# Performance work log

Measured on AMD Instinct MI355X. Metric: run time of the kernel, lower is better.

## Reference

```python
import jax, jax.numpy as jnp
import numpy as np

B, DIM, H, W, NH, WS = 128, 768, 16, 16, 12, 16
N = H * W  # 256, equals window_size**2


def setup_inputs() -> dict:
    key = jax.random.key(0)
    ks = jax.random.split(key, 8)
    s = 0.02  # small init scale for params
    return {
        "x": jax.random.normal(ks[0], (B, DIM, H, W), dtype=jnp.float32),
        "face_priors": jax.random.uniform(ks[1], (B, N, N), dtype=jnp.float32),
        "qkv_w": jax.random.normal(ks[2], (3 * DIM, DIM), dtype=jnp.float32) * s,
        "qkv_b": jax.random.normal(ks[3], (3 * DIM,), dtype=jnp.float32) * s,
        "rel_table": jax.random.normal(ks[4], ((2 * WS - 1) * (2 * WS - 1), NH), dtype=jnp.float32) * s,
        "face_prior": jax.random.normal(ks[5], (1, NH, N, N), dtype=jnp.float32) * s,
        "proj_w": jax.random.normal(ks[6], (DIM, DIM), dtype=jnp.float32) * s,
        "proj_b": jax.random.normal(ks[7], (DIM,), dtype=jnp.float32) * s,
    }


def _relative_position_bias(rel_table, h, w):
    # Static index computation (h, w are Python ints under jit).
    coords = jnp.stack(jnp.meshgrid(jnp.arange(h), jnp.arange(w), indexing="ij"))  # [2,h,w]
    flat = coords.reshape(2, -1)                     # [2, N]
    rel = flat[:, :, None] - flat[:, None, :]        # [2, N, N]
    idx = (rel[0] + h - 1) * (2 * w - 1) + (rel[1] + w - 1)  # [N, N]
    return rel_table[idx].transpose(2, 0, 1)         # [nh, N, N]


def reference(x, face_priors, qkv_w, qkv_b, rel_table, face_prior, proj_w, proj_b):
    b, c, h, w = x.shape
    n = h * w
    nh = face_prior.shape[1]
    hd = c // nh
    scale = hd ** -0.5

    x_flat = x.reshape(b, c, n).transpose(0, 2, 1)   # [B, N, C]
    qkv = (x_flat @ qkv_w.T + qkv_b).reshape(b, n, 3, nh, hd).transpose(2, 0, 3, 1, 4)
    q, k, v = qkv[0], qkv[1], qkv[2]                 # each [B, nh, N, hd]

    attn = jnp.einsum("bhnd,bhmd->bhnm", q, k) * scale
    attn = attn + face_prior + _relative_position_bias(rel_table, h, w)[None]
    attn = attn * face_priors[:, None]               # broadcast over heads
    attn = jax.nn.softmax(attn, axis=-1)

    out = jnp.einsum("bhnm,bhmd->bhnd", attn, v)     # [B, nh, N, hd]
    out = out.transpose(0, 2, 1, 3).reshape(b, n, c)
    out = out @ proj_w.T + proj_b                    # [B, N, C]
    return out.transpose(0, 2, 1).reshape(b, c, h, w)
```

## Files before the change

### kernel.cpp

```cpp
#include <hip/hip_runtime.h>

#define B_   128
#define DIM_ 768
#define NH_  12
#define HD_  64
#define N_   256

using half8 = __attribute__((ext_vector_type(8))) _Float16;
using half4 = __attribute__((ext_vector_type(4))) _Float16;
using f32x4 = __attribute__((ext_vector_type(4))) float;
typedef unsigned short u16;
typedef unsigned int   u32;

#define GLDS16(srcp, dstp) \
    __builtin_amdgcn_global_load_lds( \
        (const __attribute__((address_space(1))) void*)(srcp), \
        (__attribute__((address_space(3))) void*)(dstp), 16, 0, 0)

__device__ __forceinline__ int xcd_chunked(int orig, int nwg) {
    int xcd = orig & 7, loc = orig >> 3;
    int qq = nwg >> 3, rr = nwg & 7;
    return (xcd < rr ? xcd * (qq + 1) : rr * (qq + 1) + (xcd - rr) * qq) + loc;
}

__global__ __launch_bounds__(256) void bias16_kernel(
    const float* __restrict__ face_prior, const float* __restrict__ rel_table,
    _Float16* __restrict__ b16)
{
    int gid = blockIdx.x * 256 + threadIdx.x;
    int idx = gid * 2;
    union { _Float16 s[2]; u32 u; } P;
    #pragma unroll
    for (int j = 0; j < 2; ++j) {
        int id = idx + j;
        int m = id & 255;
        int n = (id >> 8) & 255;
        int h = id >> 16;
        int rn = n >> 4, cn = n & 15;
        int rm = m >> 4, cm = m & 15;
        int ridx = (rn - rm + 15) * 31 + (cn - cm + 15);
        P.s[j] = (_Float16)(face_prior[id] + rel_table[ridx * NH_ + h]);
    }
    *(u32*)(b16 + idx) = P.u;
}

__global__ __launch_bounds__(256) void conv_f32_f16(
    const float* __restrict__ in, _Float16* __restrict__ o16, int n8)
{
    int i = blockIdx.x * 256 + threadIdx.x;
    if (i >= n8) return;
    float4 a = *(const float4*)(in + (size_t)i * 8);
    float4 b = *(const float4*)(in + (size_t)i * 8 + 4);
    float v[8] = {a.x, a.y, a.z, a.w, b.x, b.y, b.z, b.w};
    union { _Float16 s[8]; uint4 q; } H;
    #pragma unroll
    for (int j = 0; j < 8; ++j) H.s[j] = (_Float16)v[j];
    *(uint4*)(o16 + (size_t)i * 8) = H.q;
}

__global__ __launch_bounds__(256) void conv_w_f16_staged(
    const float* __restrict__ in, _Float16* __restrict__ o16, int nchunk)
{
    int gid = blockIdx.x * 256 + threadIdx.x;
    if (gid >= nchunk) return;
    int t   = gid / 12288;
    int rem = gid % 12288;
    int ks  = rem >> 9;
    int c   = rem & 511;
    int mtb = c >> 6, kgrp = (c >> 4) & 3, r16 = c & 15;
    int srow = t * 128 + mtb * 16 + r16;
    int sk   = ks * 32 + kgrp * 8;
    float4 a = *(const float4*)(in + (size_t)srow * DIM_ + sk);
    float4 b = *(const float4*)(in + (size_t)srow * DIM_ + sk + 4);
    float v[8] = {a.x, a.y, a.z, a.w, b.x, b.y, b.z, b.w};
    union { _Float16 s[8]; uint4 q; } H;
    #pragma unroll
    for (int j = 0; j < 8; ++j) H.s[j] = (_Float16)v[j];
    *(uint4*)(o16 + (size_t)gid * 8) = H.q;
}

__global__ __launch_bounds__(256) void conv_qw_staged(
    const float* __restrict__ in, _Float16* __restrict__ o16, int nchunk)
{
    int gid = blockIdx.x * 256 + threadIdx.x;
    if (gid >= nchunk) return;
    int t   = gid / 24576;
    int rem = gid % 24576;
    int ks  = rem >> 10;
    int c   = rem & 1023;
    int mtb = c >> 6, kg = (c >> 4) & 3, r16 = c & 15;
    int srow = t * 256 + mtb * 16 + r16;
    int sk   = ks * 32 + kg * 8;
    float4 a = *(const float4*)(in + (size_t)srow * DIM_ + sk);
    float4 b = *(const float4*)(in + (size_t)srow * DIM_ + sk + 4);
    float v[8] = {a.x, a.y, a.z, a.w, b.x, b.y, b.z, b.w};
    union { _Float16 s[8]; uint4 q; } H;
    #pragma unroll
    for (int j = 0; j < 8; ++j) H.s[j] = (_Float16)v[j];
    *(uint4*)(o16 + (size_t)gid * 8) = H.q;
}

__global__ __launch_bounds__(256) void conv_transpose_x_f16(
    const float* __restrict__ x, _Float16* __restrict__ xa)
{
    __shared__ float T[64][65];
    const int b = blockIdx.z, k0 = blockIdx.x * 64, n0 = blockIdx.y * 64;
    const int t = threadIdx.x;
    const float* xb = x + (size_t)b * DIM_ * N_;
    {
        int nn = t & 63, kg = t >> 6;
        #pragma unroll
        for (int r = 0; r < 16; ++r) {
            int kk = r * 4 + kg;
            T[kk][nn] = xb[(size_t)(k0 + kk) * N_ + n0 + nn];
        }
    }
    __syncthreads();
    {
        int kk2 = (t & 31) * 2, ng = t >> 5;
        #pragma unroll
        for (int r = 0; r < 8; ++r) {
            int nn = r * 8 + ng;
            union { _Float16 s[2]; u32 u; } P;
            P.s[0] = (_Float16)T[kk2][nn];
            P.s[1] = (_Float16)T[kk2 + 1][nn];
            int n = n0 + nn, k = k0 + kk2;
            int ks = k >> 5, kg = (k >> 3) & 3, koff = k & 7;
            int mtb = n >> 4, r16 = n & 15;
            size_t o = (((size_t)b * 24 + ks) * 1024
                        + mtb * 64 + kg * 16 + r16) * 8 + koff;
            *(u32*)(xa + o) = P.u;
        }
    }
}

__global__ __launch_bounds__(512) void qkv_gemm(
    const _Float16* __restrict__ w16, const _Float16* __restrict__ x16,
    const float* __restrict__ bvec,
    _Float16* __restrict__ q16, _Float16* __restrict__ k16,
    _Float16* __restrict__ v16,
    int b0, int cb)
{
    extern __shared__ _Float16 lds[];

    const int tid  = threadIdx.x;
    const int lane = tid & 63;
    const int wv   = tid >> 6;
    const int wr   = wv >> 2;
    const int wc   = wv & 3;

    const int wg = xcd_chunked(blockIdx.x, cb * 9);
    const int by = wg % 9;
    const int bl = wg / 9;
    const int b  = b0 + bl;

    const _Float16* wbase = w16 + (size_t)by * 24 * 8192;
    const _Float16* xbase = x16 + (size_t)b  * 24 * 8192;

    f32x4 acc[8][4];
    #pragma unroll
    for (int i = 0; i < 8; ++i)
        #pragma unroll
        for (int j = 0; j < 4; ++j)
            acc[i][j] = (f32x4){0.f, 0.f, 0.f, 0.f};

    const int sbase = wv * 512;

#define STAGE_T(tt, slot) do { \
        const _Float16* ws_ = wbase + (size_t)(tt) * 8192; \
        const _Float16* xs_ = xbase + (size_t)(tt) * 8192; \
        _Float16* da_ = lds + (slot) * 8192; \
        _Float16* db_ = lds + 24576 + (slot) * 8192; \
        GLDS16(ws_ + sbase + lane * 8,        da_ + sbase); \
        GLDS16(ws_ + 4096 + sbase + lane * 8, da_ + 4096 + sbase); \
        GLDS16(xs_ + sbase + lane * 8,        db_ + sbase); \
        GLDS16(xs_ + 4096 + sbase + lane * 8, db_ + 4096 + sbase); \
    } while (0)

    STAGE_T(0, 0); STAGE_T(1, 1); STAGE_T(2, 2);

    int slot = 0;
    for (int t = 0; t < 24; ++t) {
        if (t < 22)       asm volatile("s_waitcnt vmcnt(8)" ::: "memory");
        else if (t == 22) asm volatile("s_waitcnt vmcnt(4)" ::: "memory");
        else              asm volatile("s_waitcnt vmcnt(0)" ::: "memory");
        __builtin_amdgcn_s_barrier();

        const _Float16* SAs = lds + slot * 8192;
        const _Float16* SBs = lds + 24576 + slot * 8192;
        half8 af[8];
        #pragma unroll
        for (int mt = 0; mt < 8; ++mt)
            af[mt] = *(const half8*)&SAs[((wr * 8 + mt) * 64 + lane) * 8];
        #pragma unroll
        for (int nt = 0; nt < 4; ++nt) {
            half8 bf = *(const half8*)&SBs[((wc * 4 + nt) * 64 + lane) * 8];
            #pragma unroll
            for (int mt = 0; mt < 8; ++mt)
                acc[mt][nt] = __builtin_amdgcn_mfma_f32_16x16x32_f16(af[mt], bf, acc[mt][nt], 0, 0, 0);
        }
        __builtin_amdgcn_s_barrier();

        if (t + 3 < 24) STAGE_T(t + 3, slot);
        slot = (slot == 2) ? 0 : slot + 1;
    }
#undef STAGE_T

    const int which = by / 3;
    _Float16* slab = (which == 0) ? q16 : (which == 1) ? k16 : v16;
    const int ocr0 = (by % 3) * 256 + wr * 128 + ((lane >> 4) << 2);
    const int nb   = wc * 64 + (lane & 15);

    #pragma unroll
    for (int mt = 0; mt < 8; ++mt) {
        int oc_in = ocr0 + mt * 16;
        float4 bv = *(const float4*)(bvec + which * DIM_ + oc_in);
        int hh = oc_in >> 6, d = oc_in & 63;
        size_t rowbase = ((size_t)bl * NH_ + hh) * (size_t)(N_ * HD_) + d;
        #pragma unroll
        for (int nt = 0; nt < 4; ++nt) {
            int n = nb + nt * 16;
            union { _Float16 s[4]; uint2 u; } H;
            H.s[0] = (_Float16)(acc[mt][nt][0] + bv.x);
            H.s[1] = (_Float16)(acc[mt][nt][1] + bv.y);
            H.s[2] = (_Float16)(acc[mt][nt][2] + bv.z);
            H.s[3] = (_Float16)(acc[mt][nt][3] + bv.w);
            *(uint2*)(slab + rowbase + (size_t)n * HD_) = H.u;
        }
    }
}

__global__ __launch_bounds__(256) void attn_mfma(
    const _Float16* __restrict__ q16, const _Float16* __restrict__ k16,
    const _Float16* __restrict__ v16,
    const _Float16* __restrict__ bias16, const _Float16* __restrict__ fpri16,
    _Float16* __restrict__ ao,
    int b0, int cb)
{
    extern __shared__ _Float16 ldsh[];
    _Float16* KL  = ldsh;
    _Float16* VtL = ldsh + 16384;
    const int tid  = threadIdx.x;
    const int lane = tid & 63;
    const int wv   = tid >> 6;
    _Float16* PL = ldsh + 32768 + wv * 512;

    const int bh = xcd_chunked(blockIdx.x, cb * NH_);
    const int bl = bh / NH_, h = bh % NH_;
    const int b  = b0 + bl;
    const size_t base = ((size_t)bl * NH_ + h) * (size_t)(N_ * HD_);

    const int l15 = lane & 15;
    const int lg  = lane >> 4;
    const int e   = (l15 & 3) << 1;

    #pragma unroll
    for (int s = 0; s < 8; ++s) {
        int idx = tid + s * 256;
        int r = idx >> 3, kc = (idx & 7) * 8;
        *(half8*)&KL[r * 64 + (kc ^ ((r & 7) << 3))] =
            *(const half8*)(k16 + base + (size_t)r * 64 + kc);
    }
    #pragma unroll
    for (int s = 0; s < 8; ++s) {
        int idx = tid + s * 256;
        int d = idx & 63, kkc = (idx >> 6) * 8;
        union { _Float16 sv[8]; half8 v; } t;
        #pragma unroll
        for (int j = 0; j < 8; ++j)
            t.sv[j] = v16[base + (size_t)(kkc + j) * 64 + d];
        *(half8*)&VtL[d * 256 + (kkc ^ ((d & 7) << 3))] = t.v;
    }
    __syncthreads();

    for (int qt = 0; qt < 4; ++qt) {
        const int qg = wv * 64 + qt * 16 + l15;
        const size_t qrow = base + (size_t)qg * 64;
        half8 bq[2];
        #pragma unroll
        for (int c = 0; c < 2; ++c)
            bq[c] = *(const half8*)(q16 + qrow + lg * 8 + c * 32);

        const _Float16* brow = bias16 + ((size_t)h * N_ + qg) * N_;
        const _Float16* frow = fpri16 + ((size_t)b * N_ + qg) * N_;

        float mrun = -1e30f, lrun = 0.f;
        f32x4 oacc[4];
        #pragma unroll
        for (int dt = 0; dt < 4; ++dt) oacc[dt] = (f32x4){0.f, 0.f, 0.f, 0.f};

        for (int ch = 0; ch < 2; ++ch) {
            f32x4 sacc[8];
            #pragma unroll
            for (int kt = 0; kt < 8; ++kt) {
                f32x4 sa = (f32x4){0.f, 0.f, 0.f, 0.f};
                int kr = ch * 128 + kt * 16 + l15;
                #pragma unroll
                for (int c = 0; c < 2; ++c) {
                    int kc = lg * 8 + c * 32;
                    half8 ah = *(const half8*)&KL[kr * 64 + (kc ^ ((kr & 7) << 3))];
                    sa = __builtin_amdgcn_mfma_f32_16x16x32_f16(ah, bq[c], sa, 0, 0, 0);
                }
                half4 bsv = *(const half4*)(brow + ch * 128 + kt * 16 + lg * 4);
                half4 fsv = *(const half4*)(frow + ch * 128 + kt * 16 + lg * 4);
                sacc[kt][0] = (sa[0] * 0.125f + (float)bsv[0]) * (float)fsv[0];
                sacc[kt][1] = (sa[1] * 0.125f + (float)bsv[1]) * (float)fsv[1];
                sacc[kt][2] = (sa[2] * 0.125f + (float)bsv[2]) * (float)fsv[2];
                sacc[kt][3] = (sa[3] * 0.125f + (float)bsv[3]) * (float)fsv[3];
            }

            float cmax = -1e30f;
            #pragma unroll
            for (int kt = 0; kt < 8; ++kt)
                cmax = fmaxf(cmax, fmaxf(fmaxf(sacc[kt][0], sacc[kt][1]),
                                         fmaxf(sacc[kt][2], sacc[kt][3])));
            cmax = fmaxf(cmax, __shfl_xor(cmax, 16));
            cmax = fmaxf(cmax, __shfl_xor(cmax, 32));
            float mnew = fmaxf(mrun, cmax);
            float corr = __expf(mrun - mnew);
            mrun = mnew;
            float csum = 0.f;
            #pragma unroll
            for (int kt = 0; kt < 8; ++kt) {
                #pragma unroll
                for (int j = 0; j < 4; ++j) {
                    float p = __expf(sacc[kt][j] - mnew);
                    sacc[kt][j] = p;
                    csum += p;
                }
            }
            csum += __shfl_xor(csum, 16);
            csum += __shfl_xor(csum, 32);
            lrun = lrun * corr + csum;
            #pragma unroll
            for (int dt = 0; dt < 4; ++dt) {
                oacc[dt][0] *= corr; oacc[dt][1] *= corr;
                oacc[dt][2] *= corr; oacc[dt][3] *= corr;
            }

            #pragma unroll
            for (int c2 = 0; c2 < 4; ++c2) {
                #pragma unroll
                for (int t = 0; t < 2; ++t) {
                    int kt = c2 * 2 + t;
                    union { _Float16 s[4]; uint2 u; } pw;
                    pw.s[0] = (_Float16)sacc[kt][0];
                    pw.s[1] = (_Float16)sacc[kt][1];
                    pw.s[2] = (_Float16)sacc[kt][2];
                    pw.s[3] = (_Float16)sacc[kt][3];
                    int u = (4 * t + lg) ^ e;
                    *(uint2*)&PL[l15 * 32 + u * 4] = pw.u;
                }
                half8 bp = *(const half8*)&PL[l15 * 32 + ((2 * lg) ^ e) * 4];
                int kc2 = ch * 128 + c2 * 32 + lg * 8;
                #pragma unroll
                for (int dt = 0; dt < 4; ++dt) {
                    int dr = dt * 16 + l15;
                    half8 av = *(const half8*)&VtL[dr * 256 + (kc2 ^ ((dr & 7) << 3))];
                    oacc[dt] = __builtin_amdgcn_mfma_f32_16x16x32_f16(av, bp, oacc[dt], 0, 0, 0);
                }
            }
        }

        float inv = 1.f / lrun;
        const int hf  = qg >> 7, mtb = (qg >> 4) & 7, r16 = qg & 15;
        #pragma unroll
        for (int dt = 0; dt < 4; ++dt) {
            int k = h * 64 + dt * 16 + lg * 4;
            int ks = k >> 5, kgrp = (k >> 3) & 3, koff = k & 7;
            size_t off = ((((size_t)(bl * 2 + hf) * 24 + ks) * 512)
                          + mtb * 64 + kgrp * 16 + r16) * 8 + koff;
            union { _Float16 s[4]; uint2 u; } H;
            #pragma unroll
            for (int j = 0; j < 4; ++j)
                H.s[j] = (_Float16)(oacc[dt][j] * inv);
            *(uint2*)(ao + off) = H.u;
        }
    }
}

__global__ __launch_bounds__(256) void proj_gemm(
    const _Float16* __restrict__ wst, const _Float16* __restrict__ ao,
    const float* __restrict__ bvec, float* __restrict__ outp,
    int b0, int cb)
{
    __shared__ __align__(16) _Float16 SW[4096], SX[4096];

    const int tid  = threadIdx.x;
    const int lane = tid & 63;
    const int wv   = tid >> 6;
    const int wr   = wv >> 1;
    const int wc   = wv & 1;

    const int wg = xcd_chunked(blockIdx.x, cb * 12);
    const int by = wg % 6;
    const int bx = wg / 6;
    const int bl = bx >> 1, half = bx & 1;
    const int b  = b0 + bl;

    const size_t wq0 = (size_t)by * 24 * 4096;
    const size_t xq0 = ((size_t)bl * 2 + half) * 24 * 4096;

    f32x4 acc[4][4];
    #pragma unroll
    for (int i = 0; i < 4; ++i)
        #pragma unroll
        for (int j = 0; j < 4; ++j)
            acc[i][j] = (f32x4){0.f, 0.f, 0.f, 0.f};

    const int d0 = wv * 512;

    for (int ks = 0; ks < 24; ++ks) {
        const size_t wq = wq0 + (size_t)ks * 4096 + d0;
        const size_t xq = xq0 + (size_t)ks * 4096 + d0;
        #pragma unroll
        for (int s = 0; s < 2; ++s) {
            GLDS16(wst + wq + s * 2048 + lane * 8, &SW[d0 + s * 2048]);
            GLDS16(ao  + xq + s * 2048 + lane * 8, &SX[d0 + s * 2048]);
        }
        __syncthreads();

        half8 ah[4];
        #pragma unroll
        for (int mt = 0; mt < 4; ++mt)
            ah[mt] = *(const half8*)&SW[((wr * 4 + mt) * 64 + lane) * 8];
        #pragma unroll
        for (int nt = 0; nt < 4; ++nt) {
            half8 bh = *(const half8*)&SX[((wc * 4 + nt) * 64 + lane) * 8];
            #pragma unroll
            for (int mt = 0; mt < 4; ++mt)
                acc[mt][nt] = __builtin_amdgcn_mfma_f32_16x16x32_f16(ah[mt], bh, acc[mt][nt], 0, 0, 0);
        }
        __syncthreads();
    }

    const int ocb = by * 128 + wr * 64 + (lane >> 4) * 4;
    const int nb  = half * 128 + wc * 64 + (lane & 15);

    #pragma unroll
    for (int mt = 0; mt < 4; ++mt) {
        int oc = ocb + mt * 16;
        float4 bv = *(const float4*)(bvec + oc);
        float* obase = outp + (size_t)b * DIM_ * N_ + (size_t)oc * N_;
        #pragma unroll
        for (int nt = 0; nt < 4; ++nt) {
            int n = nb + nt * 16;
            obase[0 * N_ + n] = acc[mt][nt][0] + bv.x;
            obase[1 * N_ + n] = acc[mt][nt][1] + bv.y;
            obase[2 * N_ + n] = acc[mt][nt][2] + bv.z;
            obase[3 * N_ + n] = acc[mt][nt][3] + bv.w;
        }
    }
}

extern "C" void kernel_launch(void* const* d_in, const int* in_sizes, int n_in,
                              void* d_out, int out_size, void* d_ws, size_t ws_size,
                              hipStream_t stream)
{
    const float* x           = (const float*)d_in[0];
    const float* face_priors = (const float*)d_in[1];
    const float* qkv_w       = (const float*)d_in[2];
    const float* qkv_b       = (const float*)d_in[3];
    const float* rel_table   = (const float*)d_in[4];
    const float* face_prior  = (const float*)d_in[5];
    const float* proj_w      = (const float*)d_in[6];
    const float* proj_b      = (const float*)d_in[7];
    float* out = (float*)d_out;

    _Float16* b16   = (_Float16*)d_ws;
    _Float16* fp16p = b16 + (size_t)NH_ * N_ * N_;
    _Float16* xa16  = fp16p + (size_t)B_ * N_ * N_;
    _Float16* qw16  = xa16 + (size_t)B_ * N_ * DIM_;
    _Float16* pw16  = qw16 + (size_t)3 * DIM_ * DIM_;
    _Float16* cbase = pw16 + (size_t)DIM_ * DIM_;

    const size_t PERSIST = 2ull * (NH_ * N_ * N_ + (size_t)B_ * N_ * N_
                         + (size_t)B_ * N_ * DIM_ + 4ull * DIM_ * DIM_);
    int CB = 1;
    const int cands[] = {128, 64, 32, 16, 8, 4, 2, 1};
    for (int ci = 0; ci < 8; ++ci) {
        if (PERSIST + (size_t)cands[ci] * 1572864ull <= ws_size) { CB = cands[ci]; break; }
    }
    const size_t SL = (size_t)CB * NH_ * N_ * HD_;
    _Float16* q16b = cbase;
    _Float16* k16b = q16b + SL;
    _Float16* v16b = k16b + SL;
    _Float16* aob  = v16b + SL;

    hipFuncSetAttribute((const void*)attn_mfma,
                        hipFuncAttributeMaxDynamicSharedMemorySize, 69632);
    hipFuncSetAttribute((const void*)qkv_gemm,
                        hipFuncAttributeMaxDynamicSharedMemorySize, 98304);

    bias16_kernel<<<(NH_ * N_ * N_ / 2) / 256, 256, 0, stream>>>(face_prior, rel_table, b16);
    conv_f32_f16<<<((B_ * N_ * N_ / 8) + 255) / 256, 256, 0, stream>>>(face_priors, fp16p, B_ * N_ * N_ / 8);
    conv_qw_staged<<<(9 * 24576 + 255) / 256, 256, 0, stream>>>(qkv_w, qw16, 9 * 24576);
    conv_w_f16_staged<<<(6 * 12288 + 255) / 256, 256, 0, stream>>>(proj_w, pw16, 6 * 12288);
    conv_transpose_x_f16<<<dim3(12, 4, B_), 256, 0, stream>>>(x, xa16);

    for (int b0 = 0; b0 < B_; b0 += CB) {
        qkv_gemm<<<CB * 9, 512, 98304, stream>>>(
            qw16, xa16, qkv_b, q16b, k16b, v16b, b0, CB);

        attn_mfma<<<CB * NH_, 256, 69632, stream>>>(
            q16b, k16b, v16b, b16, fp16p, aob, b0, CB);

        proj_gemm<<<CB * 12, 256, 0, stream>>>(
            pw16, aob, proj_b, out, b0, CB);
    }
}
```

Before: 387.9 us.

## Restructure QKV GEMM pipeline into double-buffered 64-wide K steps with interleaved prefetch

The QKV GEMM main loop changes from a triple-buffered 32-wide K stage to a double-buffered 64-wide K stage, with half as many iterations and barriers per tile. The async global-to-LDS loads for stage u+2 are now spread between the MFMA groups, and MFMA blocks are wrapped in s_setprio. The aim is fewer barrier stalls and better overlap of loads with compute. In exchange, LDS use rises to 128 KB, per-nt barriers are added, and the slot being refilled must not be read by a lagging wave, so correctness depends on the barrier placement.

```diff
diff --git a/kernel.cpp b/kernel.cpp
--- a/kernel.cpp
+++ b/kernel.cpp
@@ -164,47 +164,55 @@
         for (int j = 0; j < 4; ++j)
             acc[i][j] = (f32x4){0.f, 0.f, 0.f, 0.f};
 
-    const int sbase = wv * 512;
-
-#define STAGE_T(tt, slot) do { \
-        const _Float16* ws_ = wbase + (size_t)(tt) * 8192; \
-        const _Float16* xs_ = xbase + (size_t)(tt) * 8192; \
-        _Float16* da_ = lds + (slot) * 8192; \
-        _Float16* db_ = lds + 24576 + (slot) * 8192; \
-        GLDS16(ws_ + sbase + lane * 8,        da_ + sbase); \
-        GLDS16(ws_ + 4096 + sbase + lane * 8, da_ + 4096 + sbase); \
-        GLDS16(xs_ + sbase + lane * 8,        db_ + sbase); \
-        GLDS16(xs_ + 4096 + sbase + lane * 8, db_ + 4096 + sbase); \
-    } while (0)
-
-    STAGE_T(0, 0); STAGE_T(1, 1); STAGE_T(2, 2);
-
-    int slot = 0;
-    for (int t = 0; t < 24; ++t) {
-        if (t < 22)       asm volatile("s_waitcnt vmcnt(8)" ::: "memory");
-        else if (t == 22) asm volatile("s_waitcnt vmcnt(4)" ::: "memory");
-        else              asm volatile("s_waitcnt vmcnt(0)" ::: "memory");
+    const int sb = wv * 512;
+
+#define SGA(u, s, j) GLDS16(wbase + (size_t)(u) * 16384 + (j) * 4096 + sb + lane * 8, \
+                            lds + (s) * 16384 + (j) * 4096 + sb)
+#define SGB(u, s, j) GLDS16(xbase + (size_t)(u) * 16384 + (j) * 4096 + sb + lane * 8, \
+                            lds + 32768 + (s) * 16384 + (j) * 4096 + sb)
+
+    SGA(0, 0, 0); SGA(0, 0, 1); SGA(0, 0, 2); SGA(0, 0, 3);
+    SGB(0, 0, 0); SGB(0, 0, 1); SGB(0, 0, 2); SGB(0, 0, 3);
+    SGA(1, 1, 0); SGA(1, 1, 1); SGA(1, 1, 2); SGA(1, 1, 3);
+    SGB(1, 1, 0); SGB(1, 1, 1); SGB(1, 1, 2); SGB(1, 1, 3);
+
+    for (int u = 0; u < 12; ++u) {
+        const int sl = u & 1;
+        if (u < 11) asm volatile("s_waitcnt vmcnt(8)" ::: "memory");
+        else        asm volatile("s_waitcnt vmcnt(0)" ::: "memory");
         __builtin_amdgcn_s_barrier();
-
-        const _Float16* SAs = lds + slot * 8192;
-        const _Float16* SBs = lds + 24576 + slot * 8192;
-        half8 af[8];
-        #pragma unroll
-        for (int mt = 0; mt < 8; ++mt)
-            af[mt] = *(const half8*)&SAs[((wr * 8 + mt) * 64 + lane) * 8];
+        __builtin_amdgcn_sched_barrier(0);
+
+        const _Float16* SA = lds + sl * 16384;
+        const _Float16* SB = lds + 32768 + sl * 16384;
+
+        half8 af[8][2];
+        #pragma unroll
+        for (int mt = 0; mt < 8; ++mt) {
+            af[mt][0] = *(const half8*)&SA[((wr * 8 + mt) * 64 + lane) * 8];
+            af[mt][1] = *(const half8*)&SA[8192 + ((wr * 8 + mt) * 64 + lane) * 8];
+        }
+
+        const bool pre = (u + 2 < 12);
         #pragma unroll
         for (int nt = 0; nt < 4; ++nt) {
-            half8 bf = *(const half8*)&SBs[((wc * 4 + nt) * 64 + lane) * 8];
-            #pragma unroll
-            for (int mt = 0; mt < 8; ++mt)
-                acc[mt][nt] = __builtin_amdgcn_mfma_f32_16x16x32_f16(af[mt], bf, acc[mt][nt], 0, 0, 0);
-        }
-        __builtin_amdgcn_s_barrier();
-
-        if (t + 3 < 24) STAGE_T(t + 3, slot);
-        slot = (slot == 2) ? 0 : slot + 1;
-    }
-#undef STAGE_T
+            if (nt == 1 && pre) { SGA(u + 2, sl, 0); SGA(u + 2, sl, 1); }
+            if (nt == 2 && pre) { SGA(u + 2, sl, 2); SGA(u + 2, sl, 3); }
+            half8 bf0 = *(const half8*)&SB[((wc * 4 + nt) * 64 + lane) * 8];
+            half8 bf1 = *(const half8*)&SB[8192 + ((wc * 4 + nt) * 64 + lane) * 8];
+            __builtin_amdgcn_s_setprio(1);
+            #pragma unroll
+            for (int mt = 0; mt < 8; ++mt) {
+                acc[mt][nt] = __builtin_amdgcn_mfma_f32_16x16x32_f16(af[mt][0], bf0, acc[mt][nt], 0, 0, 0);
+                acc[mt][nt] = __builtin_amdgcn_mfma_f32_16x16x32_f16(af[mt][1], bf1, acc[mt][nt], 0, 0, 0);
+            }
+            __builtin_amdgcn_s_setprio(0);
+            __builtin_amdgcn_s_barrier();
+        }
+        if (pre) { SGB(u + 2, sl, 0); SGB(u + 2, sl, 1); SGB(u + 2, sl, 2); SGB(u + 2, sl, 3); }
+    }
+#undef SGA
+#undef SGB
 
     const int which = by / 3;
     _Float16* slab = (which == 0) ? q16 : (which == 1) ? k16 : v16;
@@ -490,7 +498,7 @@
     hipFuncSetAttribute((const void*)attn_mfma,
                         hipFuncAttributeMaxDynamicSharedMemorySize, 69632);
     hipFuncSetAttribute((const void*)qkv_gemm,
-                        hipFuncAttributeMaxDynamicSharedMemorySize, 98304);
+                        hipFuncAttributeMaxDynamicSharedMemorySize, 131072);
 
     bias16_kernel<<<(NH_ * N_ * N_ / 2) / 256, 256, 0, stream>>>(face_prior, rel_table, b16);
     conv_f32_f16<<<((B_ * N_ * N_ / 8) + 255) / 256, 256, 0, stream>>>(face_priors, fp16p, B_ * N_ * N_ / 8);
@@ -499,7 +507,7 @@
     conv_transpose_x_f16<<<dim3(12, 4, B_), 256, 0, stream>>>(x, xa16);
 
     for (int b0 = 0; b0 < B_; b0 += CB) {
-        qkv_gemm<<<CB * 9, 512, 98304, stream>>>(
+        qkv_gemm<<<CB * 9, 512, 131072, stream>>>(
             qw16, xa16, qkv_b, q16b, k16b, v16b, b0, CB);
 
         attn_mfma<<<CB * NH_, 256, 69632, stream>>>(
```

After: 389.7 us. About the same (+0.5%).
